# Kernel optimization log

Measured on AMD Instinct MI355X. Metric: run time of the kernel, lower is better.

The kernel has to match this reference:

```python
import jax, jax.numpy as jnp
import numpy as np

D = 1024      # input_dim / hidden_size
H = 16        # n_heads
HD = D // H   # head_size = 64
F = 4096      # mlp_dim
EPS = 1e-6


def setup_inputs() -> dict:
    key = jax.random.key(0)
    ks = jax.random.split(key, 16)
    s = 0.02
    inp = {
        "x": jax.random.normal(ks[0], (4, 2048, D), dtype=jnp.float32),
        # attention params (torch Linear: y = x @ W.T + b; we store W as [out,in])
        "Wq": jax.random.normal(ks[1], (D, D), dtype=jnp.float32) * s,
        "bq": jax.random.normal(ks[2], (D,), dtype=jnp.float32) * s,
        "Wk": jax.random.normal(ks[3], (D, D), dtype=jnp.float32) * s,
        "bk": jax.random.normal(ks[4], (D,), dtype=jnp.float32) * s,
        "Wv": jax.random.normal(ks[5], (D, D), dtype=jnp.float32) * s,
        "bv": jax.random.normal(ks[6], (D,), dtype=jnp.float32) * s,
        "Wo": jax.random.normal(ks[7], (D, D), dtype=jnp.float32) * s,
        "bo": jax.random.normal(ks[8], (D,), dtype=jnp.float32) * s,
        # MLP params
        "W1": jax.random.normal(ks[9], (F, D), dtype=jnp.float32) * s,
        "b1": jax.random.normal(ks[10], (F,), dtype=jnp.float32) * s,
        "W2": jax.random.normal(ks[11], (D, F), dtype=jnp.float32) * s,
        "b2": jax.random.normal(ks[12], (D,), dtype=jnp.float32) * s,
        # LayerNorm params
        "ln1_g": jnp.ones((D,), dtype=jnp.float32),
        "ln1_b": jnp.zeros((D,), dtype=jnp.float32),
        "ln2_g": jnp.ones((D,), dtype=jnp.float32),
        "ln2_b": jnp.zeros((D,), dtype=jnp.float32),
    }
    return inp


def _layernorm(x, g, b):
    mu = jnp.mean(x, axis=-1, keepdims=True)
    var = jnp.mean(jnp.square(x - mu), axis=-1, keepdims=True)
    return (x - mu) * jax.lax.rsqrt(var + EPS) * g + b


def reference(x, Wq, bq, Wk, bk, Wv, bv, Wo, bo, W1, b1, W2, b2,
              ln1_g, ln1_b, ln2_g, ln2_b):
    B, S, _ = x.shape
    h = x
    xn = _layernorm(x, ln1_g, ln1_b)
    # Q/K/V projections -> [B, H, S, HD]
    def split_heads(t):
        return t.reshape(B, S, H, HD).transpose(0, 2, 1, 3)
    q = split_heads(xn @ Wq.T + bq)
    k = split_heads(xn @ Wk.T + bk)
    v = split_heads(xn @ Wv.T + bv)
    scores = jnp.einsum('bhqd,bhkd->bhqk', q, k) / np.sqrt(HD).astype(np.float32)
    probs = jax.nn.softmax(scores, axis=-1)
    ctx = jnp.einsum('bhqk,bhkd->bhqd', probs, v)      # [B,H,S,HD]
    ctx = ctx.transpose(0, 2, 1, 3).reshape(B, S, D)
    attn_out = ctx @ Wo.T + bo
    x = attn_out + h
    h = x
    xn = _layernorm(x, ln2_g, ln2_b)
    y = jax.nn.gelu(xn @ W1.T + b1, approximate=False)  # torch nn.GELU() = exact erf gelu
    y = y @ W2.T + b2
    return y + h
```

## Files before the change

kernel.cpp:

```cpp
#include <hip/hip_runtime.h>
#include <hip/hip_bf16.h>
#include <math.h>

typedef __attribute__((ext_vector_type(8))) short short8;
typedef __attribute__((ext_vector_type(4))) float f32x4;

#define MFMA_BF16 __builtin_amdgcn_mfma_f32_16x16x32_bf16

__device__ __forceinline__ ushort f2bf(float f) {
  union { __hip_bfloat16 h; ushort u; } c;
  c.h = __float2bfloat16(f);
  return c.u;
}
__device__ __forceinline__ void async_cp16(const ushort* g, ushort* l) {
  __builtin_amdgcn_global_load_lds(
      (const __attribute__((address_space(1))) void*)g,
      (__attribute__((address_space(3))) void*)l, 16, 0, 0);
}

__global__ __launch_bounds__(256) void conv_all(
    const float* __restrict__ Wq, const float* __restrict__ Wk,
    const float* __restrict__ Wv, const float* __restrict__ Wo,
    const float* __restrict__ W1, const float* __restrict__ W2,
    const float* __restrict__ bq, const float* __restrict__ bk,
    const float* __restrict__ bv,
    ushort* __restrict__ wqkv, ushort* __restrict__ wo,
    ushort* __restrict__ w1, ushort* __restrict__ w2,
    float* __restrict__ bqkv) {
  int i = blockIdx.x * 256 + threadIdx.x;
  if (i < 3145728) {
    const float* src; ushort* dst; int off;
    if (i < 786432)        {
      dst = wqkv; off = i;
      if (i < 262144)      src = Wq + (size_t)i * 4;
      else if (i < 524288) src = Wk + (size_t)(i - 262144) * 4;
      else                 src = Wv + (size_t)(i - 524288) * 4;
    } else if (i < 1048576) { dst = wo; off = i - 786432;  src = Wo + (size_t)off * 4; }
    else if (i < 2097152)   { dst = w1; off = i - 1048576; src = W1 + (size_t)off * 4; }
    else                    { dst = w2; off = i - 2097152; src = W2 + (size_t)off * 4; }
    float4 v = *(const float4*)src;
    ushort4 o;
    o.x = f2bf(v.x); o.y = f2bf(v.y); o.z = f2bf(v.z); o.w = f2bf(v.w);
    ((ushort4*)dst)[off] = o;
  } else if (i < 3146496) {
    int off = i - 3145728;
    const float* src;
    if (off < 256)      src = bq + (size_t)off * 4;
    else if (off < 512) src = bk + (size_t)(off - 256) * 4;
    else                src = bv + (size_t)(off - 512) * 4;
    ((float4*)bqkv)[off] = *(const float4*)src;
  }
}

__global__ __launch_bounds__(256) void ln_kernel(const float* __restrict__ x,
    const float* __restrict__ g, const float* __restrict__ b,
    ushort* __restrict__ out) {
  const int row = blockIdx.x, t = threadIdx.x;
  float4 v = ((const float4*)(x + (size_t)row * 1024))[t];
  float s  = v.x + v.y + v.z + v.w;
  float ss = v.x*v.x + v.y*v.y + v.z*v.z + v.w*v.w;
  #pragma unroll
  for (int off = 32; off >= 1; off >>= 1) {
    s  += __shfl_xor(s, off);
    ss += __shfl_xor(ss, off);
  }
  __shared__ float red[8];
  int wv = t >> 6, ln = t & 63;
  if (ln == 0) { red[wv] = s; red[4 + wv] = ss; }
  __syncthreads();
  float S  = red[0] + red[1] + red[2] + red[3];
  float SS = red[4] + red[5] + red[6] + red[7];
  float mu  = S * (1.0f/1024.0f);
  float var = SS * (1.0f/1024.0f) - mu*mu;
  float rs  = rsqrtf(var + 1e-6f);
  float4 gv = ((const float4*)g)[t];
  float4 bv = ((const float4*)b)[t];
  ushort4 o;
  o.x = f2bf((v.x-mu)*rs*gv.x + bv.x);
  o.y = f2bf((v.y-mu)*rs*gv.y + bv.y);
  o.z = f2bf((v.z-mu)*rs*gv.z + bv.z);
  o.w = f2bf((v.w-mu)*rs*gv.w + bv.w);
  ((ushort4*)(out + (size_t)row*1024))[t] = o;
}

enum { EPI_QK = 0, EPI_VT = 1, EPI_WO = 2, EPI_GELU = 3, EPI_OUT = 4 };

template <int EPI>
__global__ __launch_bounds__(512, 2) void gemm256_kernel(const ushort* __restrict__ A,
    const ushort* __restrict__ Bw, const float* __restrict__ bias,
    void* __restrict__ outp, void* __restrict__ outp2, int K, int N, float scale) {
  __shared__ ushort As[2][256 * 64];
  __shared__ ushort Bs[2][256 * 64];
  const int t = threadIdx.x;
  const int lane = t & 63, wave = t >> 6;
  const int col = lane & 15, quad = lane >> 4;
  const int m0 = blockIdx.x * 256, n0 = blockIdx.y * 256;
  const int wm = wave >> 2, wn = wave & 3;

  f32x4 acc[8][4];
  #pragma unroll
  for (int i = 0; i < 8; i++)
    #pragma unroll
    for (int j = 0; j < 4; j++)
      acc[i][j] = (f32x4){0.f, 0.f, 0.f, 0.f};

  size_t aoff[2], boff[2];
  int d0[2];
  #pragma unroll
  for (int i = 0; i < 2; i++) {
    int c = i * 512 + t, r = c >> 3, p = c & 7;
    aoff[i] = (size_t)(m0 + r) * K + (p ^ (r & 7)) * 8;
    boff[i] = (size_t)(n0 + r) * K + (p ^ (r & 7)) * 8;
    d0[i] = c * 8;
  }
  const size_t up = (size_t)128 * K;

  const int NT = K >> 6;
  #pragma unroll
  for (int i = 0; i < 2; i++) async_cp16(A  + aoff[i],      &As[0][d0[i]]);
  #pragma unroll
  for (int i = 0; i < 2; i++) async_cp16(Bw + boff[i],      &Bs[0][d0[i]]);
  #pragma unroll
  for (int i = 0; i < 2; i++) async_cp16(A  + aoff[i] + up, &As[0][8192 + d0[i]]);
  #pragma unroll
  for (int i = 0; i < 2; i++) async_cp16(Bw + boff[i] + up, &Bs[0][8192 + d0[i]]);
  asm volatile("s_waitcnt vmcnt(4)" ::: "memory");
  __builtin_amdgcn_sched_barrier(0);
  __builtin_amdgcn_s_barrier();
  __builtin_amdgcn_sched_barrier(0);

  short8 af0[4][2], af1[4][2], bf[2][2];
  for (int kt = 0; kt < NT; kt++) {
    const int cur = kt & 1, nxt = cur ^ 1;
    const size_t ko = (size_t)(kt + 1) << 6;
    const bool more = (kt + 1 < NT);

    #pragma unroll
    for (int tml = 0; tml < 4; tml++) {
      const int row = wm * 64 + tml * 16 + col;
      #pragma unroll
      for (int c = 0; c < 2; c++)
        af0[tml][c] = *(const short8*)&As[cur][row * 64 + (((c * 4 + quad) ^ (row & 7)) * 8)];
    }
    #pragma unroll
    for (int tnl = 0; tnl < 2; tnl++) {
      const int row = wn * 32 + tnl * 16 + col;
      #pragma unroll
      for (int c = 0; c < 2; c++)
        bf[tnl][c] = *(const short8*)&Bs[cur][row * 64 + (((c * 4 + quad) ^ (row & 7)) * 8)];
    }
    if (more) {
      #pragma unroll
      for (int i = 0; i < 2; i++) async_cp16(A + aoff[i] + ko, &As[nxt][d0[i]]);
      asm volatile("s_waitcnt vmcnt(4)" ::: "memory");
    } else {
      asm volatile("s_waitcnt vmcnt(2)" ::: "memory");
    }
    __builtin_amdgcn_sched_barrier(0);
    __builtin_amdgcn_s_barrier();
    asm volatile("s_waitcnt lgkmcnt(0)" ::: "memory");
    __builtin_amdgcn_sched_barrier(0);
    __builtin_amdgcn_s_setprio(1);
    #pragma unroll
    for (int tml = 0; tml < 4; tml++)
      #pragma unroll
      for (int tnl = 0; tnl < 2; tnl++) {
        acc[tml][tnl] = MFMA_BF16(af0[tml][0], bf[tnl][0], acc[tml][tnl], 0, 0, 0);
        acc[tml][tnl] = MFMA_BF16(af0[tml][1], bf[tnl][1], acc[tml][tnl], 0, 0, 0);
      }
    __builtin_amdgcn_s_setprio(0);
    __builtin_amdgcn_sched_barrier(0);
    __builtin_amdgcn_s_barrier();
    __builtin_amdgcn_sched_barrier(0);

    #pragma unroll
    for (int tml = 0; tml < 4; tml++) {
      const int row = 128 + wm * 64 + tml * 16 + col;
      #pragma unroll
      for (int c = 0; c < 2; c++)
        af1[tml][c] = *(const short8*)&As[cur][row * 64 + (((c * 4 + quad) ^ (row & 7)) * 8)];
    }
    if (more) {
      #pragma unroll
      for (int i = 0; i < 2; i++) async_cp16(Bw + boff[i] + ko, &Bs[nxt][d0[i]]);
      asm volatile("s_waitcnt vmcnt(4)" ::: "memory");
    } else {
      asm volatile("s_waitcnt vmcnt(0)" ::: "memory");
    }
    __builtin_amdgcn_sched_barrier(0);
    __builtin_amdgcn_s_barrier();
    asm volatile("s_waitcnt lgkmcnt(0)" ::: "memory");
    __builtin_amdgcn_sched_barrier(0);
    __builtin_amdgcn_s_setprio(1);
    #pragma unroll
    for (int tml = 0; tml < 4; tml++)
      #pragma unroll
      for (int tnl = 0; tnl < 2; tnl++) {
        acc[4+tml][tnl] = MFMA_BF16(af1[tml][0], bf[tnl][0], acc[4+tml][tnl], 0, 0, 0);
        acc[4+tml][tnl] = MFMA_BF16(af1[tml][1], bf[tnl][1], acc[4+tml][tnl], 0, 0, 0);
      }
    __builtin_amdgcn_s_setprio(0);
    __builtin_amdgcn_sched_barrier(0);
    __builtin_amdgcn_s_barrier();
    __builtin_amdgcn_sched_barrier(0);

    #pragma unroll
    for (int tnl = 0; tnl < 2; tnl++) {
      const int row = 128 + wn * 32 + tnl * 16 + col;
      #pragma unroll
      for (int c = 0; c < 2; c++)
        bf[tnl][c] = *(const short8*)&Bs[cur][row * 64 + (((c * 4 + quad) ^ (row & 7)) * 8)];
    }
    if (more) {
      #pragma unroll
      for (int i = 0; i < 2; i++) async_cp16(A + aoff[i] + up + ko, &As[nxt][8192 + d0[i]]);
      asm volatile("s_waitcnt vmcnt(4)" ::: "memory");
    } else {
      asm volatile("s_waitcnt vmcnt(0)" ::: "memory");
    }
    __builtin_amdgcn_sched_barrier(0);
    __builtin_amdgcn_s_barrier();
    asm volatile("s_waitcnt lgkmcnt(0)" ::: "memory");
    __builtin_amdgcn_sched_barrier(0);
    __builtin_amdgcn_s_setprio(1);
    #pragma unroll
    for (int tml = 0; tml < 4; tml++)
      #pragma unroll
      for (int tnl = 0; tnl < 2; tnl++) {
        acc[tml][2+tnl] = MFMA_BF16(af0[tml][0], bf[tnl][0], acc[tml][2+tnl], 0, 0, 0);
        acc[tml][2+tnl] = MFMA_BF16(af0[tml][1], bf[tnl][1], acc[tml][2+tnl], 0, 0, 0);
      }
    __builtin_amdgcn_s_setprio(0);
    __builtin_amdgcn_sched_barrier(0);
    __builtin_amdgcn_s_barrier();
    __builtin_amdgcn_sched_barrier(0);

    if (more) {
      #pragma unroll
      for (int i = 0; i < 2; i++) async_cp16(Bw + boff[i] + up + ko, &Bs[nxt][8192 + d0[i]]);
      asm volatile("s_waitcnt vmcnt(4)" ::: "memory");
    } else {
      asm volatile("s_waitcnt vmcnt(0)" ::: "memory");
    }
    __builtin_amdgcn_sched_barrier(0);
    __builtin_amdgcn_s_barrier();
    asm volatile("s_waitcnt lgkmcnt(0)" ::: "memory");
    __builtin_amdgcn_sched_barrier(0);
    __builtin_amdgcn_s_setprio(1);
    #pragma unroll
    for (int tml = 0; tml < 4; tml++)
      #pragma unroll
      for (int tnl = 0; tnl < 2; tnl++) {
        acc[4+tml][2+tnl] = MFMA_BF16(af1[tml][0], bf[tnl][0], acc[4+tml][2+tnl], 0, 0, 0);
        acc[4+tml][2+tnl] = MFMA_BF16(af1[tml][1], bf[tnl][1], acc[4+tml][2+tnl], 0, 0, 0);
      }
    __builtin_amdgcn_s_setprio(0);
    __builtin_amdgcn_sched_barrier(0);
    __builtin_amdgcn_s_barrier();
    __builtin_amdgcn_sched_barrier(0);
  }

  #pragma unroll
  for (int tm = 0; tm < 8; tm++) {
    const int ha = tm >> 2, tml = tm & 3;
    #pragma unroll
    for (int tn = 0; tn < 4; tn++) {
      const int hb = tn >> 1, tnl = tn & 1;
      const int n = n0 + hb * 128 + wn * 32 + tnl * 16 + col;
      const float bn = bias[n];
      #pragma unroll
      for (int r = 0; r < 4; r++) {
        const int m = m0 + ha * 128 + wm * 64 + tml * 16 + quad * 4 + r;
        float v = acc[tm][tn][r] + bn;
        if (EPI == EPI_QK) {
          int nl = n & 1023, h = nl >> 6, hd = nl & 63;
          int bb = m >> 11, s2 = m & 2047;
          if (n < 1024)
            ((ushort*)outp)[(((size_t)(bb * 16 + h) * 2048 + s2) * 64) + hd] = f2bf(v * scale);
          else
            ((ushort*)outp2)[(((size_t)(bb * 16 + h) * 2048 + s2) * 64) + hd] = f2bf(v);
        } else {
          float u = v * 0.7978845608028654f * (1.0f + 0.044715f * v * v);
          float e = __builtin_amdgcn_exp2f(u * 2.885390081777927f);
          float th = 1.0f - 2.0f * __builtin_amdgcn_rcpf(e + 1.0f);
          ((ushort*)outp)[(size_t)m * N + n] = f2bf(0.5f * v * (1.0f + th));
        }
      }
    }
  }
}

template <int EPI>
__global__ __launch_bounds__(512, 2) void gemmH_kernel(const ushort* __restrict__ A,
    const ushort* __restrict__ Bw, const float* __restrict__ bias,
    const float* __restrict__ res, void* __restrict__ outp, int K, int N, int gx) {
  __shared__ ushort As[2][128 * 64];
  __shared__ ushort Bs[2][256 * 64];
  const int t = threadIdx.x;
  const int lane = t & 63, wave = t >> 6;
  const int col = lane & 15, quad = lane >> 4;
  const int bl = (blockIdx.x & 7) * 32 + (blockIdx.x >> 3);
  const int m0 = (bl % gx) * 128, n0 = (bl / gx) * 256;
  const int wm = wave >> 2, wn = wave & 3;

  f32x4 acc[4][4];
  #pragma unroll
  for (int i = 0; i < 4; i++)
    #pragma unroll
    for (int j = 0; j < 4; j++)
      acc[i][j] = (f32x4){0.f, 0.f, 0.f, 0.f};

  size_t aoff[2], boff[2];
  int ad0[2], bd0[2];
  #pragma unroll
  for (int i = 0; i < 2; i++) {
    int c = i * 512 + t, r = c >> 3, p = c & 7;
    aoff[i] = (size_t)(m0 + r) * K + (p ^ (r & 7)) * 8;
    boff[i] = (size_t)(n0 + r) * K + (p ^ (r & 7)) * 8;
    ad0[i] = c * 8; bd0[i] = c * 8;
  }
  const size_t upB = (size_t)128 * K;

  const int NT = K >> 6;
  #pragma unroll
  for (int i = 0; i < 2; i++) async_cp16(A  + aoff[i],       &As[0][ad0[i]]);
  #pragma unroll
  for (int i = 0; i < 2; i++) async_cp16(Bw + boff[i],       &Bs[0][bd0[i]]);
  #pragma unroll
  for (int i = 0; i < 2; i++) async_cp16(Bw + boff[i] + upB, &Bs[0][8192 + bd0[i]]);
  asm volatile("s_waitcnt vmcnt(2)" ::: "memory");
  __builtin_amdgcn_sched_barrier(0);
  __builtin_amdgcn_s_barrier();
  __builtin_amdgcn_sched_barrier(0);

  short8 af[4][2], bf[2][2];
  for (int kt = 0; kt < NT; kt++) {
    const int cur = kt & 1, nxt = cur ^ 1;
    const size_t ko = (size_t)(kt + 1) << 6;
    const bool more = (kt + 1 < NT);

    #pragma unroll
    for (int tml = 0; tml < 4; tml++) {
      const int row = wm * 64 + tml * 16 + col;
      #pragma unroll
      for (int c = 0; c < 2; c++)
        af[tml][c] = *(const short8*)&As[cur][row * 64 + (((c * 4 + quad) ^ (row & 7)) * 8)];
    }
    #pragma unroll
    for (int tnl = 0; tnl < 2; tnl++) {
      const int row = wn * 32 + tnl * 16 + col;
      #pragma unroll
      for (int c = 0; c < 2; c++)
        bf[tnl][c] = *(const short8*)&Bs[cur][row * 64 + (((c * 4 + quad) ^ (row & 7)) * 8)];
    }
    if (more) {
      #pragma unroll
      for (int i = 0; i < 2; i++) async_cp16(A  + aoff[i] + ko, &As[nxt][ad0[i]]);
      #pragma unroll
      for (int i = 0; i < 2; i++) async_cp16(Bw + boff[i] + ko, &Bs[nxt][bd0[i]]);
      asm volatile("s_waitcnt vmcnt(4)" ::: "memory");
    } else {
      asm volatile("s_waitcnt vmcnt(0)" ::: "memory");
    }
    __builtin_amdgcn_sched_barrier(0);
    __builtin_amdgcn_s_barrier();
    asm volatile("s_waitcnt lgkmcnt(0)" ::: "memory");
    __builtin_amdgcn_sched_barrier(0);
    __builtin_amdgcn_s_setprio(1);
    #pragma unroll
    for (int tml = 0; tml < 4; tml++)
      #pragma unroll
      for (int tnl = 0; tnl < 2; tnl++) {
        acc[tml][tnl] = MFMA_BF16(af[tml][0], bf[tnl][0], acc[tml][tnl], 0, 0, 0);
        acc[tml][tnl] = MFMA_BF16(af[tml][1], bf[tnl][1], acc[tml][tnl], 0, 0, 0);
      }
    __builtin_amdgcn_s_setprio(0);
    __builtin_amdgcn_sched_barrier(0);
    __builtin_amdgcn_s_barrier();
    __builtin_amdgcn_sched_barrier(0);

    #pragma unroll
    for (int tnl = 0; tnl < 2; tnl++) {
      const int rp = wn * 32 + tnl * 16 + col;
      #pragma unroll
      for (int c = 0; c < 2; c++)
        bf[tnl][c] = *(const short8*)&Bs[cur][8192 + rp * 64 + (((c * 4 + quad) ^ (rp & 7)) * 8)];
    }
    if (more) {
      #pragma unroll
      for (int i = 0; i < 2; i++) async_cp16(Bw + boff[i] + upB + ko, &Bs[nxt][8192 + bd0[i]]);
      asm volatile("s_waitcnt vmcnt(2)" ::: "memory");
    } else {
      asm volatile("s_waitcnt vmcnt(0)" ::: "memory");
    }
    __builtin_amdgcn_sched_barrier(0);
    __builtin_amdgcn_s_barrier();
    asm volatile("s_waitcnt lgkmcnt(0)" ::: "memory");
    __builtin_amdgcn_sched_barrier(0);
    __builtin_amdgcn_s_setprio(1);
    #pragma unroll
    for (int tml = 0; tml < 4; tml++)
      #pragma unroll
      for (int tnl = 0; tnl < 2; tnl++) {
        acc[tml][2+tnl] = MFMA_BF16(af[tml][0], bf[tnl][0], acc[tml][2+tnl], 0, 0, 0);
        acc[tml][2+tnl] = MFMA_BF16(af[tml][1], bf[tnl][1], acc[tml][2+tnl], 0, 0, 0);
      }
    __builtin_amdgcn_s_setprio(0);
    __builtin_amdgcn_sched_barrier(0);
    __builtin_amdgcn_s_barrier();
    __builtin_amdgcn_sched_barrier(0);
  }

  #pragma unroll
  for (int tml = 0; tml < 4; tml++) {
    #pragma unroll
    for (int tn = 0; tn < 4; tn++) {
      const int hb = tn >> 1, tnl = tn & 1;
      const int n = n0 + hb * 128 + wn * 32 + tnl * 16 + col;
      #pragma unroll
      for (int r = 0; r < 4; r++) {
        const int m = m0 + wm * 64 + tml * 16 + quad * 4 + r;
        float v = acc[tml][tn][r];
        if (EPI == EPI_VT) {
          float vv = v + bias[m];
          int h = m >> 6, hd = m & 63, bb = n >> 11, s2 = n & 2047;
          ((ushort*)outp)[((size_t)((bb * 16 + h) * 64 + hd)) * 2048 + s2] = f2bf(vv);
        } else {
          ((float*)outp)[(size_t)m * N + n] = v + bias[n] + res[(size_t)m * N + n];
        }
      }
    }
  }
}

__global__ __launch_bounds__(256) void attn_kernel(const ushort* __restrict__ Qb,
    const ushort* __restrict__ Kb, const ushort* __restrict__ Vt,
    ushort* __restrict__ ctx) {
  const int lane = threadIdx.x & 63, wave = threadIdx.x >> 6;
  const int col = lane & 15, quad = lane >> 4;
  const int bx = blockIdx.x;
  const int bh = bx & 63;
  const int qt = bx >> 6;
  const int qbase = qt * 128 + wave * 32;
  const ushort* Qh = Qb + (size_t)bh * 2048 * 64;
  const ushort* Kh = Kb + (size_t)bh * 2048 * 64;
  const ushort* Vh = Vt + (size_t)bh * 64 * 2048;

  short8 qa[2][2];
  #pragma unroll
  for (int qg = 0; qg < 2; qg++) {
    const ushort* Qr = Qh + (size_t)(qbase + qg * 16 + col) * 64 + quad * 8;
    qa[qg][0] = *(const short8*)Qr;
    qa[qg][1] = *(const short8*)(Qr + 32);
  }

  short8 ones8;
  #pragma unroll
  for (int i = 0; i < 8; i++) ones8[i] = (short)0x3F80;

  f32x4 Ot[2][4], Ol[2];
  #pragma unroll
  for (int qg = 0; qg < 2; qg++) {
    Ol[qg] = (f32x4){0.f, 0.f, 0.f, 0.f};
    #pragma unroll
    for (int dt = 0; dt < 4; dt++) Ot[qg][dt] = (f32x4){0.f, 0.f, 0.f, 0.f};
  }

  __shared__ ushort Ks[2][2][64 * 32];
  __shared__ ushort Vs[2][2][64 * 32];
  __shared__ ushort P_lds[4][16][64];

  const int lrow = lane >> 2;
  const int srow = wave * 16 + lrow;
  const int lcol = ((lane & 3) ^ ((srow >> 1) & 3)) * 8;
  const ushort* Kg = Kh + (size_t)srow * 64 + lcol;
  const ushort* Vg = Vh + (size_t)srow * 2048 + lcol;
  const int so = (wave * 16) * 32;

  const int kvswz = (col >> 1) & 3;
  const int pswz = col & 7;

  async_cp16(Kg,      &Ks[0][0][so]);
  async_cp16(Kg + 32, &Ks[0][1][so]);
  async_cp16(Vg,      &Vs[0][0][so]);
  async_cp16(Vg + 32, &Vs[0][1][so]);
  __syncthreads();

  int cur = 0;
  for (int kb = 0; kb < 2048; kb += 64) {
    if (kb + 64 < 2048) {
      const int nxt = cur ^ 1;
      async_cp16(Kg + (size_t)(kb + 64) * 64,      &Ks[nxt][0][so]);
      async_cp16(Kg + (size_t)(kb + 64) * 64 + 32, &Ks[nxt][1][so]);
      async_cp16(Vg + (kb + 64),                   &Vs[nxt][0][so]);
      async_cp16(Vg + (kb + 64) + 32,              &Vs[nxt][1][so]);
    }

    short8 kf[4][2], vf[4][2];
    #pragma unroll
    for (int kt = 0; kt < 4; kt++)
      #pragma unroll
      for (int c = 0; c < 2; c++)
        kf[kt][c] = *(const short8*)&Ks[cur][c][(kt * 16 + col) * 32 + (quad ^ kvswz) * 8];
    #pragma unroll
    for (int dt = 0; dt < 4; dt++)
      #pragma unroll
      for (int c = 0; c < 2; c++)
        vf[dt][c] = *(const short8*)&Vs[cur][c][(dt * 16 + col) * 32 + (quad ^ kvswz) * 8];

    #pragma unroll
    for (int qg = 0; qg < 2; qg++) {
      f32x4 s[4];
      __builtin_amdgcn_s_setprio(1);
      #pragma unroll
      for (int kt = 0; kt < 4; kt++) {
        s[kt] = (f32x4){0.f, 0.f, 0.f, 0.f};
        s[kt] = MFMA_BF16(kf[kt][0], qa[qg][0], s[kt], 0, 0, 0);
        s[kt] = MFMA_BF16(kf[kt][1], qa[qg][1], s[kt], 0, 0, 0);
      }
      __builtin_amdgcn_s_setprio(0);
      ushort(*P)[64] = P_lds[wave];
      #pragma unroll
      for (int kt = 0; kt < 4; kt++) {
        float p0 = __builtin_amdgcn_exp2f(s[kt][0]);
        float p1 = __builtin_amdgcn_exp2f(s[kt][1]);
        float p2 = __builtin_amdgcn_exp2f(s[kt][2]);
        float p3 = __builtin_amdgcn_exp2f(s[kt][3]);
        uint2 pk;
        asm("v_cvt_pk_bf16_f32 %0, %1, %2" : "=v"(pk.x) : "v"(p0), "v"(p1));
        asm("v_cvt_pk_bf16_f32 %0, %1, %2" : "=v"(pk.y) : "v"(p2), "v"(p3));
        *(uint2*)&P[col][(((2 * kt + (quad >> 1)) ^ pswz) * 8) + (quad & 1) * 4] = pk;
      }
      #pragma unroll
      for (int c = 0; c < 2; c++) {
        short8 pf = *(const short8*)&P_lds[wave][col][((4 * c + quad) ^ pswz) * 8];
        __builtin_amdgcn_s_setprio(1);
        #pragma unroll
        for (int dt = 0; dt < 4; dt++)
          Ot[qg][dt] = MFMA_BF16(vf[dt][c], pf, Ot[qg][dt], 0, 0, 0);
        Ol[qg] = MFMA_BF16(ones8, pf, Ol[qg], 0, 0, 0);
        __builtin_amdgcn_s_setprio(0);
      }
    }
    __syncthreads();
    cur ^= 1;
  }

  const int bb = bh >> 4, h = bh & 15;
  #pragma unroll
  for (int qg = 0; qg < 2; qg++) {
    float inv = __builtin_amdgcn_rcpf(Ol[qg][0]);
    const int q = qbase + qg * 16 + col;
    size_t base = ((size_t)(bb * 2048 + q)) * 1024 + h * 64;
    #pragma unroll
    for (int dt = 0; dt < 4; dt++) {
      ushort4 o;
      o.x = f2bf(Ot[qg][dt][0] * inv);
      o.y = f2bf(Ot[qg][dt][1] * inv);
      o.z = f2bf(Ot[qg][dt][2] * inv);
      o.w = f2bf(Ot[qg][dt][3] * inv);
      *(ushort4*)&ctx[base + dt * 16 + quad * 4] = o;
    }
  }
}

extern "C" void kernel_launch(void* const* d_in, const int* in_sizes, int n_in,
                              void* d_out, int out_size, void* d_ws, size_t ws_size,
                              hipStream_t stream) {
  const float* x     = (const float*)d_in[0];
  const float* Wq    = (const float*)d_in[1];
  const float* bq    = (const float*)d_in[2];
  const float* Wk    = (const float*)d_in[3];
  const float* bk    = (const float*)d_in[4];
  const float* Wv    = (const float*)d_in[5];
  const float* bv    = (const float*)d_in[6];
  const float* Wo    = (const float*)d_in[7];
  const float* bo    = (const float*)d_in[8];
  const float* W1    = (const float*)d_in[9];
  const float* b1    = (const float*)d_in[10];
  const float* W2    = (const float*)d_in[11];
  const float* b2    = (const float*)d_in[12];
  const float* ln1_g = (const float*)d_in[13];
  const float* ln1_b = (const float*)d_in[14];
  const float* ln2_g = (const float*)d_in[15];
  const float* ln2_b = (const float*)d_in[16];

  const size_t MB = 1ull << 20;
  char* ws = (char*)d_ws;
  ushort* Wqkv_b = (ushort*)(ws + 0 * MB);
  ushort* Wo_b   = (ushort*)(ws + 6 * MB);
  ushort* W1_b   = (ushort*)(ws + 8 * MB);
  ushort* W2_b   = (ushort*)(ws + 16 * MB);
  ushort* xn1    = (ushort*)(ws + 24 * MB);
  ushort* Qb     = (ushort*)(ws + 40 * MB);
  ushort* Kb     = (ushort*)(ws + 56 * MB);
  ushort* Vt     = (ushort*)(ws + 72 * MB);
  ushort* ctxb   = (ushort*)(ws + 88 * MB);
  float*  x2     = (float*)(ws + 104 * MB);
  ushort* xn2    = (ushort*)(ws + 136 * MB);
  ushort* y1     = (ushort*)(ws + 152 * MB);
  float*  bqkv   = (float*)(ws + 152 * MB);

  conv_all<<<12291, 256, 0, stream>>>(Wq, Wk, Wv, Wo, W1, W2, bq, bk, bv,
                                      Wqkv_b, Wo_b, W1_b, W2_b, bqkv);

  ln_kernel<<<8192, 256, 0, stream>>>(x, ln1_g, ln1_b, xn1);

  const float cs = 0.125f * 1.4426950408889634f;
  gemm256_kernel<EPI_QK><<<dim3(32, 8), 512, 0, stream>>>(
      xn1, Wqkv_b, bqkv, Qb, Kb, 1024, 2048, cs);
  gemmH_kernel<EPI_VT><<<256, 512, 0, stream>>>(
      Wqkv_b + (size_t)2048 * 1024, xn1, bqkv + 2048, nullptr, Vt, 1024, 8192, 8);

  attn_kernel<<<1024, 256, 0, stream>>>(Qb, Kb, Vt, ctxb);

  gemmH_kernel<EPI_WO><<<256, 512, 0, stream>>>(
      ctxb, Wo_b, bo, x, x2, 1024, 1024, 64);

  ln_kernel<<<8192, 256, 0, stream>>>(x2, ln2_g, ln2_b, xn2);

  gemm256_kernel<EPI_GELU><<<dim3(32, 16), 512, 0, stream>>>(
      xn2, W1_b, b1, y1, nullptr, 1024, 4096, 1.0f);
  gemmH_kernel<EPI_OUT><<<256, 512, 0, stream>>>(
      y1, W2_b, b2, x2, d_out, 4096, 1024, 64);
}
```

Measured before the change: 499.9 us.

## Drop trailing GEMM barriers and widen attention blocks to eight waves

Removes the block-wide barrier that followed each MFMA phase in both GEMM kernels, leaving one barrier per phase to cut synchronization stalls. Separately, the attention kernel now runs 512 threads per block covering 256 queries. Half the waves load K tiles and half load V tiles, so each K/V tile loaded into LDS is shared by twice as many queries. Removing the barriers risks LDS read/write races with the next async copy into the buffer being read, and the larger attention blocks halve the grid size and change occupancy.

```diff
diff --git a/kernel.cpp b/kernel.cpp
--- a/kernel.cpp
+++ b/kernel.cpp
@@ -169,9 +169,6 @@
         acc[tml][tnl] = MFMA_BF16(af0[tml][1], bf[tnl][1], acc[tml][tnl], 0, 0, 0);
       }
     __builtin_amdgcn_s_setprio(0);
-    __builtin_amdgcn_sched_barrier(0);
-    __builtin_amdgcn_s_barrier();
-    __builtin_amdgcn_sched_barrier(0);
 
     #pragma unroll
     for (int tml = 0; tml < 4; tml++) {
@@ -200,9 +197,6 @@
         acc[4+tml][tnl] = MFMA_BF16(af1[tml][1], bf[tnl][1], acc[4+tml][tnl], 0, 0, 0);
       }
     __builtin_amdgcn_s_setprio(0);
-    __builtin_amdgcn_sched_barrier(0);
-    __builtin_amdgcn_s_barrier();
-    __builtin_amdgcn_sched_barrier(0);
 
     #pragma unroll
     for (int tnl = 0; tnl < 2; tnl++) {
@@ -231,9 +225,6 @@
         acc[tml][2+tnl] = MFMA_BF16(af0[tml][1], bf[tnl][1], acc[tml][2+tnl], 0, 0, 0);
       }
     __builtin_amdgcn_s_setprio(0);
-    __builtin_amdgcn_sched_barrier(0);
-    __builtin_amdgcn_s_barrier();
-    __builtin_amdgcn_sched_barrier(0);
 
     if (more) {
       #pragma unroll
@@ -255,9 +246,6 @@
         acc[4+tml][2+tnl] = MFMA_BF16(af1[tml][1], bf[tnl][1], acc[4+tml][2+tnl], 0, 0, 0);
       }
     __builtin_amdgcn_s_setprio(0);
-    __builtin_amdgcn_sched_barrier(0);
-    __builtin_amdgcn_s_barrier();
-    __builtin_amdgcn_sched_barrier(0);
   }
 
   #pragma unroll
@@ -375,9 +363,6 @@
         acc[tml][tnl] = MFMA_BF16(af[tml][1], bf[tnl][1], acc[tml][tnl], 0, 0, 0);
       }
     __builtin_amdgcn_s_setprio(0);
-    __builtin_amdgcn_sched_barrier(0);
-    __builtin_amdgcn_s_barrier();
-    __builtin_amdgcn_sched_barrier(0);
 
     #pragma unroll
     for (int tnl = 0; tnl < 2; tnl++) {
@@ -406,9 +391,6 @@
         acc[tml][2+tnl] = MFMA_BF16(af[tml][1], bf[tnl][1], acc[tml][2+tnl], 0, 0, 0);
       }
     __builtin_amdgcn_s_setprio(0);
-    __builtin_amdgcn_sched_barrier(0);
-    __builtin_amdgcn_s_barrier();
-    __builtin_amdgcn_sched_barrier(0);
   }
 
   #pragma unroll
@@ -433,7 +415,7 @@
   }
 }
 
-__global__ __launch_bounds__(256) void attn_kernel(const ushort* __restrict__ Qb,
+__global__ __launch_bounds__(512) void attn_kernel(const ushort* __restrict__ Qb,
     const ushort* __restrict__ Kb, const ushort* __restrict__ Vt,
     ushort* __restrict__ ctx) {
   const int lane = threadIdx.x & 63, wave = threadIdx.x >> 6;
@@ -441,7 +423,7 @@
   const int bx = blockIdx.x;
   const int bh = bx & 63;
   const int qt = bx >> 6;
-  const int qbase = qt * 128 + wave * 32;
+  const int qbase = qt * 256 + wave * 32;
   const ushort* Qh = Qb + (size_t)bh * 2048 * 64;
   const ushort* Kh = Kb + (size_t)bh * 2048 * 64;
   const ushort* Vh = Vt + (size_t)bh * 64 * 2048;
@@ -468,32 +450,40 @@
 
   __shared__ ushort Ks[2][2][64 * 32];
   __shared__ ushort Vs[2][2][64 * 32];
-  __shared__ ushort P_lds[4][16][64];
+  __shared__ ushort P_lds[8][16][64];
 
   const int lrow = lane >> 2;
-  const int srow = wave * 16 + lrow;
+  const int sw = wave & 3;
+  const int srow = sw * 16 + lrow;
   const int lcol = ((lane & 3) ^ ((srow >> 1) & 3)) * 8;
   const ushort* Kg = Kh + (size_t)srow * 64 + lcol;
   const ushort* Vg = Vh + (size_t)srow * 2048 + lcol;
-  const int so = (wave * 16) * 32;
+  const int so = (sw * 16) * 32;
+  const bool kRole = (wave < 4);
 
   const int kvswz = (col >> 1) & 3;
   const int pswz = col & 7;
 
-  async_cp16(Kg,      &Ks[0][0][so]);
-  async_cp16(Kg + 32, &Ks[0][1][so]);
-  async_cp16(Vg,      &Vs[0][0][so]);
-  async_cp16(Vg + 32, &Vs[0][1][so]);
+  if (kRole) {
+    async_cp16(Kg,      &Ks[0][0][so]);
+    async_cp16(Kg + 32, &Ks[0][1][so]);
+  } else {
+    async_cp16(Vg,      &Vs[0][0][so]);
+    async_cp16(Vg + 32, &Vs[0][1][so]);
+  }
   __syncthreads();
 
   int cur = 0;
   for (int kb = 0; kb < 2048; kb += 64) {
     if (kb + 64 < 2048) {
       const int nxt = cur ^ 1;
-      async_cp16(Kg + (size_t)(kb + 64) * 64,      &Ks[nxt][0][so]);
-      async_cp16(Kg + (size_t)(kb + 64) * 64 + 32, &Ks[nxt][1][so]);
-      async_cp16(Vg + (kb + 64),                   &Vs[nxt][0][so]);
-      async_cp16(Vg + (kb + 64) + 32,              &Vs[nxt][1][so]);
+      if (kRole) {
+        async_cp16(Kg + (size_t)(kb + 64) * 64,      &Ks[nxt][0][so]);
+        async_cp16(Kg + (size_t)(kb + 64) * 64 + 32, &Ks[nxt][1][so]);
+      } else {
+        async_cp16(Vg + (kb + 64),                   &Vs[nxt][0][so]);
+        async_cp16(Vg + (kb + 64) + 32,              &Vs[nxt][1][so]);
+      }
     }
 
     short8 kf[4][2], vf[4][2];
@@ -612,7 +602,7 @@
   gemmH_kernel<EPI_VT><<<256, 512, 0, stream>>>(
       Wqkv_b + (size_t)2048 * 1024, xn1, bqkv + 2048, nullptr, Vt, 1024, 8192, 8);
 
-  attn_kernel<<<1024, 256, 0, stream>>>(Qb, Kb, Vt, ctxb);
+  attn_kernel<<<512, 512, 0, stream>>>(Qb, Kb, Vt, ctxb);
 
   gemmH_kernel<EPI_WO><<<256, 512, 0, stream>>>(
       ctxb, Wo_b, bo, x, x2, 1024, 1024, 64);
```

Result: faster. 482.4 us (-3.5%).
